# Kernel tuning notes

Hardware: AMD Instinct MI355X
Metric: run time of the kernel (lower is better)

Reference implementation:

```python
import jax, jax.numpy as jnp
import numpy as np

LAT_MIN, LAT_MAX = -90.0, 90.0
LON_MIN, LON_MAX = 0.0, 360.0
N_LEVELS = 4
N_FEAT = 2
FINEST = 0.25
BASE = 1.0
LAT_SHAPE, LON_SHAPE = 720, 1440
GEODESIC_WEIGHT = True
TABLE = (LAT_SHAPE + 1) * (LON_SHAPE + 1)  # 1038961
# corner offsets in the torch BOX_OFFSETS order: (0,0),(0,1),(1,0),(1,1)
OFFS = np.array([[0, 0], [0, 1], [1, 0], [1, 1]], dtype=np.int32)


def setup_inputs() -> dict:
    key = jax.random.key(0)
    k1, k2 = jax.random.split(key)
    B = 2_000_000
    u = jax.random.uniform(k1, (B, 2), dtype=jnp.float32)
    # lat in [-90, 90), lon in [0, 360)
    x = jnp.stack([u[:, 0] * 180.0 - 90.0, u[:, 1] * 360.0], axis=1)
    embeddings = jax.random.uniform(k2, (N_LEVELS, TABLE, N_FEAT),
                                    minval=-1e-4, maxval=1e-4, dtype=jnp.float32)
    return {"x": x, "embeddings": embeddings}


def _geodesic(lat1, lon1, lat2, lon2):
    r = jnp.pi / 180.0
    rl1, rl2 = lat1 * r, lat2 * r
    dlat = (lat2 - lat1) * r
    dlon = (lon2 - lon1) * r
    a = jnp.sin(dlat / 2) ** 2 + jnp.cos(rl1) * jnp.cos(rl2) * jnp.sin(dlon / 2) ** 2
    return 2.0 * jnp.arctan2(jnp.sqrt(a), jnp.sqrt(1.0 - a))


def reference(x, embeddings):
    box_min = jnp.array([LAT_MIN - FINEST, LON_MIN - FINEST], dtype=x.dtype)
    box_max = jnp.array([LAT_MAX + FINEST, LON_MAX + FINEST], dtype=x.dtype)
    xc = jnp.clip(x, box_min, box_max)  # clamped coords used for grid indexing
    offs = jnp.asarray(OFFS)
    outs = []
    for i in range(N_LEVELS):
        gs = BASE * (2.0 ** i)  # grid size (same for lat and lon)
        bl = jnp.floor((xc - box_min) / gs).astype(jnp.int32)  # [B,2] bottom-left idx
        gmin = bl.astype(x.dtype) * gs + box_min                # [B,2]
        gmax = gmin + gs
        width = int(np.floor(LON_SHAPE / gs))
        # 4 corner flat indices: lat_idx * width + lon_idx -> [B,4]
        idx = (bl[:, 0:1] + offs[None, :, 0]) * width + (bl[:, 1:2] + offs[None, :, 1])
        e = embeddings[i][idx]  # gather: [B,4,F]
        if GEODESIC_WEIGHT:
            wlat = _geodesic(gmin[:, 0], gmin[:, 1], x[:, 0], gmin[:, 1]) / \
                   _geodesic(gmin[:, 0], gmin[:, 1], gmax[:, 0], gmin[:, 1])
            wlon = _geodesic(gmin[:, 0], x[:, 1], gmin[:, 0], gmax[:, 1]) / \
                   _geodesic(gmin[:, 0], gmin[:, 1], gmin[:, 0], gmax[:, 1])
        else:
            w = (x - gmin) / (gmax - gmin)
            wlat, wlon = w[:, 0], w[:, 1]
        # bilinear blend (corner order: 0=(0,0) 1=(0,1) 2=(1,0) 3=(1,1))
        c0 = e[:, 0] * (1 - wlat[:, None]) + e[:, 2] * wlat[:, None]
        c1 = e[:, 1] * (1 - wlat[:, None]) + e[:, 3] * wlat[:, None]
        outs.append(c0 * (1 - wlon[:, None]) + c1 * wlon[:, None])
    return jnp.concatenate(outs, axis=-1)  # [B, N_LEVELS*N_FEAT]
```

## Files before the change

### kernel.cpp

```cpp
#include <hip/hip_runtime.h>
#include <hip/hip_fp16.h>

#define NT 256
#define PPT 4

constexpr int TABLE_SZ = 721 * 1441;

constexpr int QLAT = 181, QLON = 361;
constexpr int NCELLS = QLAT * QLON;

constexpr int LUT_OFF0 = 0, LUT_OFF1 = 181, LUT_OFF2 = 272, LUT_OFF3 = 318;
constexpr int LUT_N = 341;

typedef float v4f __attribute__((ext_vector_type(4)));
typedef float v2f __attribute__((ext_vector_type(2)));

__device__ __constant__ float c_s2_tab[4] = {0.008726535498f, 0.017452406437f,
                                             0.034899496703f, 0.069756473744f};

__global__ __launch_bounds__(256)
void build_superquad(const float* __restrict__ emb, uint4* __restrict__ sq)
{
    int c = blockIdx.x * 256 + threadIdx.x;
    if (c >= NCELLS) return;
    int la = c / QLON, lo = c - la * QLON;
    const float2* embv = (const float2*)emb;
    #pragma unroll
    for (int i = 0; i < 4; ++i) {
        const int width = 1440 >> i;
        const int ra = la >> i, co = lo >> i;
        const float2* t = embv + (size_t)i * TABLE_SZ;
        float2 e0 = t[ra * width + co];
        float2 e1 = t[ra * width + co + 1];
        float2 e2 = t[(ra + 1) * width + co];
        float2 e3 = t[(ra + 1) * width + co + 1];
        union { uint4 u; __half2 h[4]; } pk;
        pk.h[0] = __floats2half2_rn(e0.x, e0.y);
        pk.h[1] = __floats2half2_rn(e1.x, e1.y);
        pk.h[2] = __floats2half2_rn(e2.x, e2.y);
        pk.h[3] = __floats2half2_rn(e3.x, e3.y);
        sq[(size_t)c * 4 + i] = pk.u;
    }
}

__global__ __launch_bounds__(NT)
void ngp_interp_lv(const float* __restrict__ x,
                   const uint4* __restrict__ sq,
                   float* __restrict__ out,
                   int B)
{
    const float r = 0.017453292519943295f;
    const float bmin_lat = -90.25f;
    const float bmin_lon = -0.25f;
    const float bmax_lat = 90.25f, bmax_lon = 360.25f;

    const int t   = threadIdx.x;
    const int lvl = t & 3;
    const int pg  = t >> 2;
    const int pbase = blockIdx.x * ((NT / 4) * PPT) + pg;

    const float gs     = __int_as_float(0x3f800000 + (lvl << 23));
    const float inv_gs = __int_as_float(0x3f800000 - (lvl << 23));
    const int lut_off_l = (lvl >= 1 ? 181 : 0) + (lvl >= 2 ? 91 : 0)
                        + (lvl >= 3 ? 46 : 0);

    int pidx[PPT];
    v2f xp[PPT];
    #pragma unroll
    for (int k = 0; k < PPT; ++k) {
        const int p = pbase + k * (NT / 4);
        pidx[k] = p;
        const int pc = p < B ? p : B - 1;
        xp[k] = __builtin_nontemporal_load(reinterpret_cast<const v2f*>(x) + pc);
    }

    __shared__ float2 lut[LUT_N];
    for (int i = t; i < LUT_N; i += NT) {
        int lv, row;
        if (i < LUT_OFF1)      { lv = 0; row = i; }
        else if (i < LUT_OFF2) { lv = 1; row = i - LUT_OFF1; }
        else if (i < LUT_OFF3) { lv = 2; row = i - LUT_OFF2; }
        else                   { lv = 3; row = i - LUT_OFF3; }
        const float gsl = (float)(1 << lv);
        const float gmin_lat = (float)row * gsl + bmin_lat;
        const float ca = fabsf(__cosf(gmin_lat * r));
        const float z2 = ca * c_s2_tab[lv];
        const float n2 = z2 + z2 * z2 * z2 * (1.0f / 6.0f);
        lut[i] = make_float2(ca, __builtin_amdgcn_rcpf(n2));
    }
    __syncthreads();

    float vlat[PPT], vlon[PPT];
    uint4 g[PPT];
    #pragma unroll
    for (int k = 0; k < PPT; ++k) {
        const float xlat = xp[k].x;
        const float xlon = xp[k].y;
        const float xc_lat = fminf(fmaxf(xlat, bmin_lat), bmax_lat);
        const float xc_lon = fminf(fmaxf(xlon, bmin_lon), bmax_lon);
        vlat[k] = xc_lat - bmin_lat;
        vlon[k] = xc_lon - bmin_lon;
        const int cell0 = (int)floorf(vlat[k]) * QLON + (int)floorf(vlon[k]);
        g[k] = sq[(size_t)cell0 * 4 + lvl];
    }

    #pragma unroll
    for (int k = 0; k < PPT; ++k) {
        const float xlat = xp[k].x;
        const float xlon = xp[k].y;
        const float v_lat = vlat[k];
        const float v_lon = vlon[k];

        const float blat_f = floorf(v_lat * inv_gs);
        const float blon_f = floorf(v_lon * inv_gs);
        const float gmin_lat = blat_f * gs + bmin_lat;
        const float gmin_lon = blon_f * gs + bmin_lon;
        const float gmax_lon = gmin_lon + gs;
        const int bl_lat = (int)blat_f;

        union { uint4 u; __half2 h[4]; } pk;
        pk.u = g[k];
        const float2 f0 = __half22float2(pk.h[0]);
        const float2 f1 = __half22float2(pk.h[1]);
        const float2 f2 = __half22float2(pk.h[2]);
        const float2 f3 = __half22float2(pk.h[3]);
        const v2f E0 = {f0.x, f0.y}, E1 = {f1.x, f1.y};
        const v2f E2 = {f2.x, f2.y}, E3 = {f3.x, f3.y};

        const float wlat = (xlat - gmin_lat) * inv_gs;

        const float2 cl = lut[lut_off_l + bl_lat];
        const float h1 = (gmax_lon - xlon) * r * 0.5f;
        const float s1 = h1 - h1 * h1 * h1 * (1.0f / 6.0f);
        const float z1 = cl.x * s1;
        const float n1 = z1 + z1 * z1 * z1 * (1.0f / 6.0f);
        const float wlon = n1 * cl.y;

        const v2f wa = {wlat, wlat};
        const v2f wo = {wlon, wlon};
        const v2f c0 = E0 + (E2 - E0) * wa;
        const v2f c1 = E1 + (E3 - E1) * wa;
        const v2f res = c0 + (c1 - c0) * wo;

        if (pidx[k] < B) {
            v2f* op = reinterpret_cast<v2f*>(out + (size_t)pidx[k] * 8 + lvl * 2);
            __builtin_nontemporal_store(res, op);
        }
    }
}

__global__ __launch_bounds__(NT)
void ngp_interp_fb(const float* __restrict__ x,
                   const float* __restrict__ emb,
                   float* __restrict__ out,
                   int B)
{
    const float r = 0.017453292519943295f;
    const float bmin_lat = -90.25f;
    const float bmin_lon = -0.25f;

    __shared__ float2 lut[LUT_N];
    for (int t = threadIdx.x; t < LUT_N; t += NT) {
        int lvl, row;
        if (t < LUT_OFF1)      { lvl = 0; row = t; }
        else if (t < LUT_OFF2) { lvl = 1; row = t - LUT_OFF1; }
        else if (t < LUT_OFF3) { lvl = 2; row = t - LUT_OFF2; }
        else                   { lvl = 3; row = t - LUT_OFF3; }
        const float gs = (float)(1 << lvl);
        const float gmin_lat = (float)row * gs + bmin_lat;
        const float ca = fabsf(__cosf(gmin_lat * r));
        const float z2 = ca * c_s2_tab[lvl];
        const float n2 = z2 + z2 * z2 * z2 * (1.0f / 6.0f);
        lut[t] = make_float2(ca, __builtin_amdgcn_rcpf(n2));
    }
    __syncthreads();

    const int p = blockIdx.x * NT + threadIdx.x;
    if (p >= B) return;

    const v2f xp = __builtin_nontemporal_load(reinterpret_cast<const v2f*>(x) + p);
    const float xlat = xp.x;
    const float xlon = xp.y;

    const float bmax_lat = 90.25f, bmax_lon = 360.25f;
    const float xc_lat = fminf(fmaxf(xlat, bmin_lat), bmax_lat);
    const float xc_lon = fminf(fmaxf(xlon, bmin_lon), bmax_lon);
    const float v_lat = xc_lat - bmin_lat;
    const float v_lon = xc_lon - bmin_lon;

    const int lut_off[4] = {LUT_OFF0, LUT_OFF1, LUT_OFF2, LUT_OFF3};
    float o[8];

    #pragma unroll
    for (int i = 0; i < 4; ++i) {
        const float gs     = (float)(1 << i);
        const float inv_gs = 1.0f / gs;
        const int   width  = 1440 >> i;

        const float blat_f = floorf(v_lat * inv_gs);
        const float blon_f = floorf(v_lon * inv_gs);
        const float gmin_lat = blat_f * gs + bmin_lat;
        const float gmin_lon = blon_f * gs + bmin_lon;
        const float gmax_lon = gmin_lon + gs;
        const int bl_lat = (int)blat_f;
        const int bl_lon = (int)blon_f;

        const int idx00 = bl_lat * width + bl_lon;
        const float* base0 = emb + ((size_t)i * TABLE_SZ + (size_t)idx00) * 2;
        const float* base1 = base0 + (size_t)width * 2;
        v4f eA, eB;
        __builtin_memcpy(&eA, base0, 16);
        __builtin_memcpy(&eB, base1, 16);
        const v2f E0 = {eA.x, eA.y}, E1 = {eA.z, eA.w};
        const v2f E2 = {eB.x, eB.y}, E3 = {eB.z, eB.w};

        const float wlat = (xlat - gmin_lat) * inv_gs;

        const float2 cl = lut[lut_off[i] + bl_lat];
        const float h1 = (gmax_lon - xlon) * r * 0.5f;
        const float s1 = h1 - h1 * h1 * h1 * (1.0f / 6.0f);
        const float z1 = cl.x * s1;
        const float n1 = z1 + z1 * z1 * z1 * (1.0f / 6.0f);
        const float wlon = n1 * cl.y;

        const v2f wa = {wlat, wlat};
        const v2f wo = {wlon, wlon};
        const v2f c0 = E0 + (E2 - E0) * wa;
        const v2f c1 = E1 + (E3 - E1) * wa;
        const v2f res = c0 + (c1 - c0) * wo;
        o[2*i]   = res.x;
        o[2*i+1] = res.y;
    }

    v4f* op = reinterpret_cast<v4f*>(out + (size_t)p * 8);
    const v4f lo = {o[0], o[1], o[2], o[3]};
    const v4f hi = {o[4], o[5], o[6], o[7]};
    __builtin_nontemporal_store(lo, op);
    __builtin_nontemporal_store(hi, op + 1);
}

extern "C" void kernel_launch(void* const* d_in, const int* in_sizes, int n_in,
                              void* d_out, int out_size, void* d_ws, size_t ws_size,
                              hipStream_t stream)
{
    const float* x   = (const float*)d_in[0];
    const float* emb = (const float*)d_in[1];
    float* out = (float*)d_out;
    const int B = in_sizes[0] / 2;

    const size_t sq_bytes = (size_t)NCELLS * 64;
    if (ws_size >= sq_bytes) {
        uint4* sq = (uint4*)d_ws;
        build_superquad<<<(NCELLS + 255) / 256, 256, 0, stream>>>(emb, sq);
        const int pts_per_blk = (NT / 4) * PPT;
        const int grid = (B + pts_per_blk - 1) / pts_per_blk;
        ngp_interp_lv<<<grid, NT, 0, stream>>>(x, sq, out, B);
    } else {
        const int grid = (B + NT - 1) / NT;
        ngp_interp_fb<<<grid, NT, 0, stream>>>(x, emb, out, B);
    }
}
```

Baseline: 120.7 us.

## Keep coarse levels in shared memory and shrink per-cell table to two levels

The per-cell precomputed quad table now holds only levels 0 and 1 (32 bytes per cell instead of 64). Levels 2 and 3 are packed as small fp16 vertex tables that every block copies into shared memory. Each thread now handles all four levels for its own points and writes the full 8-float output row with two vector stores, instead of one thread per level. This halves the global gather traffic, at the cost of a per-block shared-memory fill (about 22 KB), more LDS reads per point, and more registers per thread.

Result: faster. 115.2 us (-4.5%).

```diff
diff --git a/kernel.cpp b/kernel.cpp
--- a/kernel.cpp
+++ b/kernel.cpp
@@ -9,7 +9,15 @@
 constexpr int QLAT = 181, QLON = 361;
 constexpr int NCELLS = QLAT * QLON;
 
-constexpr int LUT_OFF0 = 0, LUT_OFF1 = 181, LUT_OFF2 = 272, LUT_OFF3 = 318;
+constexpr int VT2_C = 92, VT2_N = 47 * 92;
+constexpr int VT3_C = 47, VT3_N = 24 * 47;
+constexpr int VT_N  = VT2_N + VT3_N;
+constexpr int VT_N4 = VT_N / 4;
+
+constexpr size_t OFF_VT  = (size_t)NCELLS * 32;
+constexpr size_t WS_NEED = OFF_VT + (size_t)VT_N * 4;
+
+constexpr int LUT_OFF1 = 181, LUT_OFF2 = 272, LUT_OFF3 = 318;
 constexpr int LUT_N = 341;
 
 typedef float v4f __attribute__((ext_vector_type(4)));
@@ -19,60 +27,76 @@
                                              0.034899496703f, 0.069756473744f};
 
 __global__ __launch_bounds__(256)
-void build_superquad(const float* __restrict__ emb, uint4* __restrict__ sq)
+void build_tables(const float* __restrict__ emb,
+                  uint4* __restrict__ sq,
+                  uint*  __restrict__ vt)
 {
-    int c = blockIdx.x * 256 + threadIdx.x;
-    if (c >= NCELLS) return;
-    int la = c / QLON, lo = c - la * QLON;
+    const int t = blockIdx.x * 256 + threadIdx.x;
     const float2* embv = (const float2*)emb;
-    #pragma unroll
-    for (int i = 0; i < 4; ++i) {
-        const int width = 1440 >> i;
-        const int ra = la >> i, co = lo >> i;
-        const float2* t = embv + (size_t)i * TABLE_SZ;
-        float2 e0 = t[ra * width + co];
-        float2 e1 = t[ra * width + co + 1];
-        float2 e2 = t[(ra + 1) * width + co];
-        float2 e3 = t[(ra + 1) * width + co + 1];
-        union { uint4 u; __half2 h[4]; } pk;
-        pk.h[0] = __floats2half2_rn(e0.x, e0.y);
-        pk.h[1] = __floats2half2_rn(e1.x, e1.y);
-        pk.h[2] = __floats2half2_rn(e2.x, e2.y);
-        pk.h[3] = __floats2half2_rn(e3.x, e3.y);
-        sq[(size_t)c * 4 + i] = pk.u;
+    if (t < NCELLS) {
+        const int la = t / QLON, lo = t - la * QLON;
+        #pragma unroll
+        for (int i = 0; i < 2; ++i) {
+            const int width = 1440 >> i;
+            const int ra = la >> i, co = lo >> i;
+            const float2* tb = embv + (size_t)i * TABLE_SZ;
+            const float2 e0 = tb[ra * width + co];
+            const float2 e1 = tb[ra * width + co + 1];
+            const float2 e2 = tb[(ra + 1) * width + co];
+            const float2 e3 = tb[(ra + 1) * width + co + 1];
+            union { uint4 u; __half2 h[4]; } pk;
+            pk.h[0] = __floats2half2_rn(e0.x, e0.y);
+            pk.h[1] = __floats2half2_rn(e1.x, e1.y);
+            pk.h[2] = __floats2half2_rn(e2.x, e2.y);
+            pk.h[3] = __floats2half2_rn(e3.x, e3.y);
+            sq[(size_t)t * 2 + i] = pk.u;
+        }
+    } else {
+        const int u = t - NCELLS;
+        if (u < VT_N) {
+            float2 e;
+            if (u < VT2_N) {
+                const int rr = u / VT2_C, cc = u - rr * VT2_C;
+                e = embv[(size_t)2 * TABLE_SZ + rr * 360 + cc];
+            } else {
+                const int v = u - VT2_N;
+                const int rr = v / VT3_C, cc = v - rr * VT3_C;
+                e = embv[(size_t)3 * TABLE_SZ + rr * 180 + cc];
+            }
+            union { uint uu; __half2 h; } pk;
+            pk.h = __floats2half2_rn(e.x, e.y);
+            vt[u] = pk.uu;
+        }
     }
 }
 
 __global__ __launch_bounds__(NT)
-void ngp_interp_lv(const float* __restrict__ x,
-                   const uint4* __restrict__ sq,
-                   float* __restrict__ out,
-                   int B)
+void ngp_interp(const float* __restrict__ x,
+                const uint4* __restrict__ sq,
+                const uint4* __restrict__ vtq,
+                float* __restrict__ out,
+                int B)
 {
     const float r = 0.017453292519943295f;
     const float bmin_lat = -90.25f;
     const float bmin_lon = -0.25f;
     const float bmax_lat = 90.25f, bmax_lon = 360.25f;
 
-    const int t   = threadIdx.x;
-    const int lvl = t & 3;
-    const int pg  = t >> 2;
-    const int pbase = blockIdx.x * ((NT / 4) * PPT) + pg;
-
-    const float gs     = __int_as_float(0x3f800000 + (lvl << 23));
-    const float inv_gs = __int_as_float(0x3f800000 - (lvl << 23));
-    const int lut_off_l = (lvl >= 1 ? 181 : 0) + (lvl >= 2 ? 91 : 0)
-                        + (lvl >= 3 ? 46 : 0);
+    const int t = threadIdx.x;
+    const int base = blockIdx.x * (NT * PPT) + t;
 
     int pidx[PPT];
     v2f xp[PPT];
     #pragma unroll
     for (int k = 0; k < PPT; ++k) {
-        const int p = pbase + k * (NT / 4);
+        const int p = base + k * NT;
         pidx[k] = p;
         const int pc = p < B ? p : B - 1;
         xp[k] = __builtin_nontemporal_load(reinterpret_cast<const v2f*>(x) + pc);
     }
+
+    __shared__ uint4 s_vt[VT_N4];
+    for (int i = t; i < VT_N4; i += NT) s_vt[i] = vtq[i];
 
     __shared__ float2 lut[LUT_N];
     for (int i = t; i < LUT_N; i += NT) {
@@ -90,8 +114,11 @@
     }
     __syncthreads();
 
+    const uint* vt2 = (const uint*)s_vt;
+    const uint* vt3 = vt2 + VT2_N;
+
     float vlat[PPT], vlon[PPT];
-    uint4 g[PPT];
+    uint4 g0[PPT], g1[PPT];
     #pragma unroll
     for (int k = 0; k < PPT; ++k) {
         const float xlat = xp[k].x;
@@ -101,7 +128,9 @@
         vlat[k] = xc_lat - bmin_lat;
         vlon[k] = xc_lon - bmin_lon;
         const int cell0 = (int)floorf(vlat[k]) * QLON + (int)floorf(vlon[k]);
-        g[k] = sq[(size_t)cell0 * 4 + lvl];
+        const uint4* cp = sq + (size_t)cell0 * 2;
+        g0[k] = cp[0];
+        g1[k] = cp[1];
     }
 
     #pragma unroll
@@ -111,40 +140,82 @@
         const float v_lat = vlat[k];
         const float v_lon = vlon[k];
 
-        const float blat_f = floorf(v_lat * inv_gs);
-        const float blon_f = floorf(v_lon * inv_gs);
-        const float gmin_lat = blat_f * gs + bmin_lat;
-        const float gmin_lon = blon_f * gs + bmin_lon;
-        const float gmax_lon = gmin_lon + gs;
-        const int bl_lat = (int)blat_f;
-
-        union { uint4 u; __half2 h[4]; } pk;
-        pk.u = g[k];
-        const float2 f0 = __half22float2(pk.h[0]);
-        const float2 f1 = __half22float2(pk.h[1]);
-        const float2 f2 = __half22float2(pk.h[2]);
-        const float2 f3 = __half22float2(pk.h[3]);
-        const v2f E0 = {f0.x, f0.y}, E1 = {f1.x, f1.y};
-        const v2f E2 = {f2.x, f2.y}, E3 = {f3.x, f3.y};
-
-        const float wlat = (xlat - gmin_lat) * inv_gs;
-
-        const float2 cl = lut[lut_off_l + bl_lat];
-        const float h1 = (gmax_lon - xlon) * r * 0.5f;
-        const float s1 = h1 - h1 * h1 * h1 * (1.0f / 6.0f);
-        const float z1 = cl.x * s1;
-        const float n1 = z1 + z1 * z1 * z1 * (1.0f / 6.0f);
-        const float wlon = n1 * cl.y;
-
-        const v2f wa = {wlat, wlat};
-        const v2f wo = {wlon, wlon};
-        const v2f c0 = E0 + (E2 - E0) * wa;
-        const v2f c1 = E1 + (E3 - E1) * wa;
-        const v2f res = c0 + (c1 - c0) * wo;
+        float o[8];
+
+        auto weights = [&](float gs, float inv_gs, int lut_base,
+                           float blat_f, float blon_f,
+                           float& wlat, float& wlon) {
+            const float gmin_lat = blat_f * gs + bmin_lat;
+            const float gmin_lon = blon_f * gs + bmin_lon;
+            const float gmax_lon = gmin_lon + gs;
+            wlat = (xlat - gmin_lat) * inv_gs;
+            const float2 cl = lut[lut_base + (int)blat_f];
+            const float h1 = (gmax_lon - xlon) * r * 0.5f;
+            const float s1 = h1 - h1 * h1 * h1 * (1.0f / 6.0f);
+            const float z1 = cl.x * s1;
+            const float n1 = z1 + z1 * z1 * z1 * (1.0f / 6.0f);
+            wlon = n1 * cl.y;
+        };
+        auto bilerp = [](float2 f0, float2 f1, float2 f2, float2 f3,
+                         float wlat, float wlon, float* dst) {
+            const v2f E0 = {f0.x, f0.y}, E1 = {f1.x, f1.y};
+            const v2f E2 = {f2.x, f2.y}, E3 = {f3.x, f3.y};
+            const v2f wa = {wlat, wlat};
+            const v2f wo = {wlon, wlon};
+            const v2f c0 = E0 + (E2 - E0) * wa;
+            const v2f c1 = E1 + (E3 - E1) * wa;
+            const v2f res = c0 + (c1 - c0) * wo;
+            dst[0] = res.x; dst[1] = res.y;
+        };
+
+        #pragma unroll
+        for (int i = 0; i < 2; ++i) {
+            const float gs = (float)(1 << i);
+            const float inv_gs = 1.0f / gs;
+            const float blat_f = floorf(v_lat * inv_gs);
+            const float blon_f = floorf(v_lon * inv_gs);
+            float wlat, wlon;
+            weights(gs, inv_gs, i == 0 ? 0 : LUT_OFF1, blat_f, blon_f, wlat, wlon);
+            union { uint4 u; __half2 h[4]; } pk;
+            pk.u = i == 0 ? g0[k] : g1[k];
+            bilerp(__half22float2(pk.h[0]), __half22float2(pk.h[1]),
+                   __half22float2(pk.h[2]), __half22float2(pk.h[3]),
+                   wlat, wlon, &o[2 * i]);
+        }
+
+        {
+            const float blat_f = floorf(v_lat * 0.25f);
+            const float blon_f = floorf(v_lon * 0.25f);
+            float wlat, wlon;
+            weights(4.0f, 0.25f, LUT_OFF2, blat_f, blon_f, wlat, wlon);
+            const int i2 = (int)blat_f * VT2_C + (int)blon_f;
+            union { uint uu; __half2 h; } a0, a1, a2, a3;
+            a0.uu = vt2[i2];            a1.uu = vt2[i2 + 1];
+            a2.uu = vt2[i2 + VT2_C];    a3.uu = vt2[i2 + VT2_C + 1];
+            bilerp(__half22float2(a0.h), __half22float2(a1.h),
+                   __half22float2(a2.h), __half22float2(a3.h),
+                   wlat, wlon, &o[4]);
+        }
+        {
+            const float blat_f = floorf(v_lat * 0.125f);
+            const float blon_f = floorf(v_lon * 0.125f);
+            float wlat, wlon;
+            weights(8.0f, 0.125f, LUT_OFF3, blat_f, blon_f, wlat, wlon);
+            const int i3 = (int)blat_f * VT3_C + (int)blon_f;
+            union { uint uu; __half2 h; } a0, a1, a2, a3;
+            a0.uu = vt3[i3];            a1.uu = vt3[i3 + 1];
+            a2.uu = vt3[i3 + VT3_C];    a3.uu = vt3[i3 + VT3_C + 1];
+            bilerp(__half22float2(a0.h), __half22float2(a1.h),
+                   __half22float2(a2.h), __half22float2(a3.h),
+                   wlat, wlon, &o[6]);
+        }
 
         if (pidx[k] < B) {
-            v2f* op = reinterpret_cast<v2f*>(out + (size_t)pidx[k] * 8 + lvl * 2);
-            __builtin_nontemporal_store(res, op);
+            v4f* op = reinterpret_cast<v4f*>(out + (size_t)pidx[k] * 8);
+            const v4f lo = {o[0], o[1], o[2], o[3]};
+            const v4f hi = {o[4], o[5], o[6], o[7]};
+            __builtin_nontemporal_store(lo, op);
+            __builtin_nontemporal_store(hi, op + 1);
         }
     }
 }
@@ -188,7 +259,7 @@
     const float v_lat = xc_lat - bmin_lat;
     const float v_lon = xc_lon - bmin_lon;
 
-    const int lut_off[4] = {LUT_OFF0, LUT_OFF1, LUT_OFF2, LUT_OFF3};
+    const int lut_off[4] = {0, LUT_OFF1, LUT_OFF2, LUT_OFF3};
     float o[8];
 
     #pragma unroll
@@ -248,13 +319,14 @@
     float* out = (float*)d_out;
     const int B = in_sizes[0] / 2;
 
-    const size_t sq_bytes = (size_t)NCELLS * 64;
-    if (ws_size >= sq_bytes) {
+    if (ws_size >= WS_NEED) {
         uint4* sq = (uint4*)d_ws;
-        build_superquad<<<(NCELLS + 255) / 256, 256, 0, stream>>>(emb, sq);
-        const int pts_per_blk = (NT / 4) * PPT;
+        uint*  vt = (uint*)((char*)d_ws + OFF_VT);
+        const int nbuild = NCELLS + VT_N;
+        build_tables<<<(nbuild + 255) / 256, 256, 0, stream>>>(emb, sq, vt);
+        const int pts_per_blk = NT * PPT;
         const int grid = (B + pts_per_blk - 1) / pts_per_blk;
-        ngp_interp_lv<<<grid, NT, 0, stream>>>(x, sq, out, B);
+        ngp_interp<<<grid, NT, 0, stream>>>(x, sq, (const uint4*)vt, out, B);
     } else {
         const int grid = (B + NT - 1) / NT;
         ngp_interp_fb<<<grid, NT, 0, stream>>>(x, emb, out, B);
```
